# Optimization experiments

Measured on AMD Instinct MI355X. Metric: run time of the kernel, lower is better.

The kernel has to match this reference:

```python
import jax, jax.numpy as jnp
import numpy as np

K = 4          # non-zeros kept per block
BLOCK = 8      # block size along last dim (block_dim = -1)


def _block_topk_mask(score):
    # score last dim is a multiple of BLOCK; block_dim == -1 so no transpose needed.
    s = score.reshape(-1, BLOCK)                       # [n_blocks, BLOCK]
    # argsort ascending; drop the (BLOCK-K) smallest entries per block
    idx = jnp.argsort(s, axis=1)[:, : BLOCK - K]       # [n_blocks, BLOCK-K]
    rows = jnp.arange(s.shape[0])[:, None]
    mask = jnp.ones_like(s).at[rows, idx].set(0.0)     # scatter zeros at pruned idx
    return mask.reshape(score.shape)


def setup_inputs() -> dict:
    key = jax.random.key(0)
    k1, k2 = jax.random.split(key)
    x = jax.random.normal(k1, (8192, 8192), dtype=jnp.float32)
    score = jax.random.normal(k2, (8192, 8192), dtype=jnp.float32)  # learned score param
    return {"x": x, "score": score}


def reference(x, score):
    # Sparsify.forward (training, BlockTopK): mask = sparseness.get_mask(score); out = x * mask
    mask = _block_topk_mask(score)
    return x * mask
```

## Files before the change

### kernel.cpp

```cpp
#include <hip/hip_runtime.h>


__global__ __launch_bounds__(256) void sparsify_topk_kernel(
    const float4* __restrict__ x4,
    const float4* __restrict__ s4,
    float4* __restrict__ o4,
    int nblk)
{
    int b = blockIdx.x * blockDim.x + threadIdx.x;
    if (b >= nblk) return;

    float4 sa = s4[2 * b];
    float4 sb = s4[2 * b + 1];
    float4 xa = x4[2 * b];
    float4 xb = x4[2 * b + 1];

    float s[8] = {sa.x, sa.y, sa.z, sa.w, sb.x, sb.y, sb.z, sb.w};
    float v[8] = {xa.x, xa.y, xa.z, xa.w, xb.x, xb.y, xb.z, xb.w};
    float o[8];

#pragma unroll
    for (int i = 0; i < 8; ++i) {
        int rank = 0;
#pragma unroll
        for (int j = 0; j < 8; ++j) {
            rank += (s[j] < s[i]) || ((s[j] == s[i]) && (j < i));
        }
        o[i] = (rank >= 4) ? v[i] : 0.0f;
    }

    o4[2 * b]     = make_float4(o[0], o[1], o[2], o[3]);
    o4[2 * b + 1] = make_float4(o[4], o[5], o[6], o[7]);
}

extern "C" void kernel_launch(void* const* d_in, const int* in_sizes, int n_in,
                              void* d_out, int out_size, void* d_ws, size_t ws_size,
                              hipStream_t stream) {
    const float4* x4 = (const float4*)d_in[0];
    const float4* s4 = (const float4*)d_in[1];
    float4* o4 = (float4*)d_out;

    int n = in_sizes[0];
    int nblk = n / 8;

    const int threads = 256;
    int grid = (nblk + threads - 1) / threads;
    sparsify_topk_kernel<<<grid, threads, 0, stream>>>(x4, s4, o4, nblk);
}
```

Baseline: 569.3 us.

## Split each 8-element block across lane pairs with shuffles for coalesced float4 access

Each thread now handles one float4 (half of a block) and gets the other half's scores from its neighbour lane via __shfl_xor, so adjacent lanes read adjacent 16-byte chunks. This replaces the old pattern where each thread read two consecutive float4s. Each thread also processes two float4s spaced 256 apart, so it has more loads in flight. Ties are broken by giving the odd (upper-half) lane the higher index. The kernel is memory bound, so the gain depends on whether coalescing and memory-level parallelism improve; the shuffles and added compares cost extra instructions.

```diff
diff --git a/kernel.cpp b/kernel.cpp
--- a/kernel.cpp
+++ b/kernel.cpp
@@ -1,36 +1,52 @@
 #include <hip/hip_runtime.h>
 
+
+__device__ __forceinline__ float4 topk_half(float4 s, float4 xv, bool upper) {
+    float4 t;
+    t.x = __shfl_xor(s.x, 1);
+    t.y = __shfl_xor(s.y, 1);
+    t.z = __shfl_xor(s.z, 1);
+    t.w = __shfl_xor(s.w, 1);
+
+    float ss[4] = {s.x, s.y, s.z, s.w};
+    float tt[4] = {t.x, t.y, t.z, t.w};
+    float xx[4] = {xv.x, xv.y, xv.z, xv.w};
+    float oo[4];
+
+#pragma unroll
+    for (int i = 0; i < 4; ++i) {
+        int rank = 0;
+#pragma unroll
+        for (int j = 0; j < 4; ++j) {
+            rank += (ss[j] < ss[i]) || ((ss[j] == ss[i]) && (j < i));
+            rank += (tt[j] < ss[i]) || (upper && (tt[j] == ss[i]));
+        }
+        oo[i] = (rank >= 4) ? xx[i] : 0.0f;
+    }
+    return make_float4(oo[0], oo[1], oo[2], oo[3]);
+}
 
 __global__ __launch_bounds__(256) void sparsify_topk_kernel(
     const float4* __restrict__ x4,
     const float4* __restrict__ s4,
     float4* __restrict__ o4,
-    int nblk)
+    int nf)
 {
-    int b = blockIdx.x * blockDim.x + threadIdx.x;
-    if (b >= nblk) return;
+    int f0 = blockIdx.x * 512 + threadIdx.x;
+    int f1 = f0 + 256;
+    bool upper = (threadIdx.x & 1);
 
-    float4 sa = s4[2 * b];
-    float4 sb = s4[2 * b + 1];
-    float4 xa = x4[2 * b];
-    float4 xb = x4[2 * b + 1];
-
-    float s[8] = {sa.x, sa.y, sa.z, sa.w, sb.x, sb.y, sb.z, sb.w};
-    float v[8] = {xa.x, xa.y, xa.z, xa.w, xb.x, xb.y, xb.z, xb.w};
-    float o[8];
-
-#pragma unroll
-    for (int i = 0; i < 8; ++i) {
-        int rank = 0;
-#pragma unroll
-        for (int j = 0; j < 8; ++j) {
-            rank += (s[j] < s[i]) || ((s[j] == s[i]) && (j < i));
-        }
-        o[i] = (rank >= 4) ? v[i] : 0.0f;
+    if (f1 < nf) {
+        float4 s0 = s4[f0];
+        float4 x0 = x4[f0];
+        float4 s1 = s4[f1];
+        float4 x1 = x4[f1];
+        o4[f0] = topk_half(s0, x0, upper);
+        o4[f1] = topk_half(s1, x1, upper);
+    } else {
+        if (f0 < nf) o4[f0] = topk_half(s4[f0], x4[f0], upper);
+        if (f1 < nf) o4[f1] = topk_half(s4[f1], x4[f1], upper);
     }
-
-    o4[2 * b]     = make_float4(o[0], o[1], o[2], o[3]);
-    o4[2 * b + 1] = make_float4(o[4], o[5], o[6], o[7]);
 }
 
 extern "C" void kernel_launch(void* const* d_in, const int* in_sizes, int n_in,
@@ -41,9 +57,8 @@
     float4* o4 = (float4*)d_out;
 
     int n = in_sizes[0];
-    int nblk = n / 8;
+    int nf = n / 4;
+    int grid = (nf + 511) / 512;
 
-    const int threads = 256;
-    int grid = (nblk + threads - 1) / threads;
-    sparsify_topk_kernel<<<grid, threads, 0, stream>>>(x4, s4, o4, nblk);
+    sparsify_topk_kernel<<<grid, 256, 0, stream>>>(x4, s4, o4, nf);
 }
```

Result: no change. 576.7 us (+1.3%).
